# Kernel optimization log

Measured on AMD Instinct MI355X. Metric: run time of the kernel, lower is better.

Reference implementation:

```python
import jax, jax.numpy as jnp
import numpy as np

ALPHA = 0.2        # LeakyReLU negative slope in EEGGraphAttentionLayer
NEG_BIG = -9e15    # zero_vec value used before softmax

B, N, F_IN, H = 32, 1024, 512, 512


def setup_inputs() -> dict:
    key = jax.random.key(0)
    k1, k2, k3, k4 = jax.random.split(key, 4)
    context = jax.random.normal(k1, (B, N, F_IN), dtype=jnp.float32)
    adj = jax.random.randint(k2, (B, N, N), 0, 2, dtype=jnp.int32)
    w = jax.random.normal(k3, (F_IN, H), dtype=jnp.float32) * (1.414 / np.sqrt(F_IN))
    a = jax.random.normal(k4, (2 * H, 1), dtype=jnp.float32) * (1.414 / np.sqrt(2 * H))
    return {"context": context, "adj": adj, "w": w, "a": a}


def reference(context, adj, w, a):
    # context: (B, N, F), adj: (B, N, N), w: (F, H), a: (2H, 1)
    # All num_pers=16 heads share the identical att module, so the mean over
    # num_pers of identical tensors equals a single application (same math).
    context = context.reshape(adj.shape[0], adj.shape[1], -1)
    Wh = jnp.einsum('bnf,fh->bnh', context, w)            # (B, N, H)
    a1, a2 = a[:H, 0], a[H:, 0]                            # (H,), (H,)
    f1 = Wh @ a1                                           # (B, N) -> source index i
    f2 = Wh @ a2                                           # (B, N) -> target index j
    # e[b,i,j] = leakyrelu(f1[b,i] + f2[b,j]); avoids the explicit N x N x 2H tensor
    e = jax.nn.leaky_relu(f1[:, :, None] + f2[:, None, :], negative_slope=ALPHA)
    e = jnp.where(adj > 0, e, NEG_BIG)
    attention = jax.nn.softmax(e, axis=-1)                 # softmax over dim=1 of (N,N)
    # F.dropout is a no-op in eval mode; epsilon=None, ctx_mask=None paths skipped.
    return jax.nn.softplus(attention)
```

## Files before the change

kernel.cpp:

```cpp
#include <hip/hip_runtime.h>
#include <math.h>

#define ALPHA 0.2f

constexpr int B = 32, N = 1024, F_IN = 512, H = 512;

typedef float f32x4 __attribute__((ext_vector_type(4)));

__global__ __launch_bounds__(64) void u_kernel(const float* __restrict__ w,
                                               const float* __restrict__ a,
                                               float* __restrict__ u) {
    const int f = blockIdx.x;
    const int l = threadIdx.x;
    const float* wrow = w + (size_t)f * H;
    float s1 = 0.f, s2 = 0.f;
#pragma unroll
    for (int it = 0; it < H / 64; ++it) {
        const int h = l + it * 64;
        const float wv = wrow[h];
        s1 += wv * a[h];
        s2 += wv * a[h + H];
    }
#pragma unroll
    for (int off = 32; off > 0; off >>= 1) {
        s1 += __shfl_xor(s1, off, 64);
        s2 += __shfl_xor(s2, off, 64);
    }
    if (l == 0) { u[f] = s1; u[f + F_IN] = s2; }
}

__global__ __launch_bounds__(256) void f_kernel(const float* __restrict__ ctx,
                                                const float* __restrict__ u,
                                                float* __restrict__ f1,
                                                float* __restrict__ f2) {
    const int wave = threadIdx.x >> 6;
    const int lane = threadIdx.x & 63;
    const int row  = blockIdx.x * 4 + wave;

    const float4* u1p = (const float4*)u;
    const float4* u2p = (const float4*)(u + F_IN);
    const float4 u1a = u1p[lane * 2],     u1b = u1p[lane * 2 + 1];
    const float4 u2a = u2p[lane * 2],     u2b = u2p[lane * 2 + 1];

    const float4* c4 = (const float4*)(ctx + (size_t)row * F_IN);
    const float4 ca = c4[lane * 2], cb = c4[lane * 2 + 1];

    float s1 = ca.x * u1a.x + ca.y * u1a.y + ca.z * u1a.z + ca.w * u1a.w
             + cb.x * u1b.x + cb.y * u1b.y + cb.z * u1b.z + cb.w * u1b.w;
    float s2 = ca.x * u2a.x + ca.y * u2a.y + ca.z * u2a.z + ca.w * u2a.w
             + cb.x * u2b.x + cb.y * u2b.y + cb.z * u2b.z + cb.w * u2b.w;

#pragma unroll
    for (int off = 32; off > 0; off >>= 1) {
        s1 += __shfl_xor(s1, off, 64);
        s2 += __shfl_xor(s2, off, 64);
    }
    if (lane == 0) { f1[row] = s1; f2[row] = s2; }
}

__device__ __forceinline__ float softplus01(float z) {
    const float z2 = z * z;
    const float t  = fmaf(z2, -5.2083335e-3f, 0.125f);
    return fmaf(z2, t, fmaf(z, 0.5f, 0.69314718f));
}

__global__ __launch_bounds__(256) void attn_kernel(const int* __restrict__ adj,
                                                   const float* __restrict__ f1,
                                                   const float* __restrict__ f2,
                                                   float* __restrict__ out) {
    const int wave = threadIdx.x >> 6;
    const int lane = threadIdx.x & 63;
    const int row  = blockIdx.x * 4 + wave;
    const int b    = row >> 10;

    const int4*   arow = (const int4*)(adj + (size_t)row * N);
    const float4* f2b  = (const float4*)(f2 + (size_t)b * N);
    const float   fi   = f1[row];

    int4   am[4];
    float4 fv[4];
#pragma unroll
    for (int k = 0; k < 4; ++k) {
        am[k] = arow[k * 64 + lane];
        fv[k] = f2b[k * 64 + lane];
    }

    float p[16];
    float s = 0.f;
#pragma unroll
    for (int k = 0; k < 4; ++k) {
        const float f0 = fv[k].x, f1v = fv[k].y, f2v = fv[k].z, f3v = fv[k].w;
        float e0 = fi + f0;  e0 = e0 > 0.f ? e0 : ALPHA * e0;
        float e1 = fi + f1v; e1 = e1 > 0.f ? e1 : ALPHA * e1;
        float e2 = fi + f2v; e2 = e2 > 0.f ? e2 : ALPHA * e2;
        float e3 = fi + f3v; e3 = e3 > 0.f ? e3 : ALPHA * e3;
        const float q0 = (am[k].x > 0) ? __expf(e0) : 0.f;
        const float q1 = (am[k].y > 0) ? __expf(e1) : 0.f;
        const float q2 = (am[k].z > 0) ? __expf(e2) : 0.f;
        const float q3 = (am[k].w > 0) ? __expf(e3) : 0.f;
        p[k * 4 + 0] = q0; p[k * 4 + 1] = q1; p[k * 4 + 2] = q2; p[k * 4 + 3] = q3;
        s += (q0 + q1) + (q2 + q3);
    }

#pragma unroll
    for (int off = 32; off > 0; off >>= 1)
        s += __shfl_xor(s, off, 64);
    const float inv = (s > 0.f) ? (1.0f / s) : 0.f;

    f32x4* orow = (f32x4*)(out + (size_t)row * N);
#pragma unroll
    for (int k = 0; k < 4; ++k) {
        f32x4 o;
        o.x = softplus01(p[k * 4 + 0] * inv);
        o.y = softplus01(p[k * 4 + 1] * inv);
        o.z = softplus01(p[k * 4 + 2] * inv);
        o.w = softplus01(p[k * 4 + 3] * inv);
        __builtin_nontemporal_store(o, orow + k * 64 + lane);
    }
}

extern "C" void kernel_launch(void* const* d_in, const int* in_sizes, int n_in,
                              void* d_out, int out_size, void* d_ws, size_t ws_size,
                              hipStream_t stream) {
    const float* ctx = (const float*)d_in[0];
    const int*   adj = (const int*)d_in[1];
    const float* w   = (const float*)d_in[2];
    const float* a   = (const float*)d_in[3];
    float* out = (float*)d_out;

    float* u  = (float*)d_ws;
    float* f1 = u + 2 * F_IN;
    float* f2 = f1 + B * N;

    u_kernel<<<F_IN, 64, 0, stream>>>(w, a, u);
    f_kernel<<<(B * N) / 4, 256, 0, stream>>>(ctx, u, f1, f2);
    attn_kernel<<<(B * N) / 4, 256, 0, stream>>>(adj, f1, f2, out);
}
```

Measured before the change: 59.65 us.

## Fuse f-projection and attention kernels into persistent grid with global barrier

```diff
diff --git a/kernel.cpp b/kernel.cpp
--- a/kernel.cpp
+++ b/kernel.cpp
@@ -4,12 +4,18 @@
 #define ALPHA 0.2f
 
 constexpr int B = 32, N = 1024, F_IN = 512, H = 512;
+constexpr int GRID = 512, BLK = 256;
+constexpr int ROWS_PER_BLOCK = (B * N) / GRID;
+constexpr int ROWS_PER_WAVE  = ROWS_PER_BLOCK / 4;
 
 typedef float f32x4 __attribute__((ext_vector_type(4)));
 
+
 __global__ __launch_bounds__(64) void u_kernel(const float* __restrict__ w,
                                                const float* __restrict__ a,
-                                               float* __restrict__ u) {
+                                               float* __restrict__ u,
+                                               int* __restrict__ bar) {
+    if (blockIdx.x == 0 && threadIdx.x == 0) { bar[0] = 0; bar[1] = 0; }
     const int f = blockIdx.x;
     const int l = threadIdx.x;
     const float* wrow = w + (size_t)f * H;
@@ -29,93 +35,114 @@
     if (l == 0) { u[f] = s1; u[f + F_IN] = s2; }
 }
 
-__global__ __launch_bounds__(256) void f_kernel(const float* __restrict__ ctx,
-                                                const float* __restrict__ u,
-                                                float* __restrict__ f1,
-                                                float* __restrict__ f2) {
-    const int wave = threadIdx.x >> 6;
-    const int lane = threadIdx.x & 63;
-    const int row  = blockIdx.x * 4 + wave;
-
-    const float4* u1p = (const float4*)u;
-    const float4* u2p = (const float4*)(u + F_IN);
-    const float4 u1a = u1p[lane * 2],     u1b = u1p[lane * 2 + 1];
-    const float4 u2a = u2p[lane * 2],     u2b = u2p[lane * 2 + 1];
-
-    const float4* c4 = (const float4*)(ctx + (size_t)row * F_IN);
-    const float4 ca = c4[lane * 2], cb = c4[lane * 2 + 1];
-
-    float s1 = ca.x * u1a.x + ca.y * u1a.y + ca.z * u1a.z + ca.w * u1a.w
-             + cb.x * u1b.x + cb.y * u1b.y + cb.z * u1b.z + cb.w * u1b.w;
-    float s2 = ca.x * u2a.x + ca.y * u2a.y + ca.z * u2a.z + ca.w * u2a.w
-             + cb.x * u2b.x + cb.y * u2b.y + cb.z * u2b.z + cb.w * u2b.w;
-
-#pragma unroll
-    for (int off = 32; off > 0; off >>= 1) {
-        s1 += __shfl_xor(s1, off, 64);
-        s2 += __shfl_xor(s2, off, 64);
-    }
-    if (lane == 0) { f1[row] = s1; f2[row] = s2; }
-}
-
 __device__ __forceinline__ float softplus01(float z) {
     const float z2 = z * z;
     const float t  = fmaf(z2, -5.2083335e-3f, 0.125f);
     return fmaf(z2, t, fmaf(z, 0.5f, 0.69314718f));
 }
 
-__global__ __launch_bounds__(256) void attn_kernel(const int* __restrict__ adj,
-                                                   const float* __restrict__ f1,
-                                                   const float* __restrict__ f2,
-                                                   float* __restrict__ out) {
+__global__ __launch_bounds__(BLK, 2) void fused_kernel(
+        const float* __restrict__ ctx, const int* __restrict__ adj,
+        const float* __restrict__ u,   float* __restrict__ f2,
+        int* __restrict__ bar,         float* __restrict__ out) {
     const int wave = threadIdx.x >> 6;
     const int lane = threadIdx.x & 63;
-    const int row  = blockIdx.x * 4 + wave;
-    const int b    = row >> 10;
+    const int baseRow = blockIdx.x * ROWS_PER_BLOCK + wave * ROWS_PER_WAVE;
 
-    const int4*   arow = (const int4*)(adj + (size_t)row * N);
-    const float4* f2b  = (const float4*)(f2 + (size_t)b * N);
-    const float   fi   = f1[row];
-
-    int4   am[4];
-    float4 fv[4];
+    float f1r[ROWS_PER_WAVE];
+    {
+        const float4* u1p = (const float4*)u;
+        const float4* u2p = (const float4*)(u + F_IN);
+        const float4 u1a = u1p[lane * 2], u1b = u1p[lane * 2 + 1];
+        const float4 u2a = u2p[lane * 2], u2b = u2p[lane * 2 + 1];
 #pragma unroll
-    for (int k = 0; k < 4; ++k) {
-        am[k] = arow[k * 64 + lane];
-        fv[k] = f2b[k * 64 + lane];
+        for (int i = 0; i < ROWS_PER_WAVE; ++i) {
+            const int row = baseRow + i;
+            const float4* c4 = (const float4*)(ctx + (size_t)row * F_IN);
+            const float4 ca = c4[lane * 2], cb = c4[lane * 2 + 1];
+            float s1 = ca.x * u1a.x + ca.y * u1a.y + ca.z * u1a.z + ca.w * u1a.w
+                     + cb.x * u1b.x + cb.y * u1b.y + cb.z * u1b.z + cb.w * u1b.w;
+            float s2 = ca.x * u2a.x + ca.y * u2a.y + ca.z * u2a.z + ca.w * u2a.w
+                     + cb.x * u2b.x + cb.y * u2b.y + cb.z * u2b.z + cb.w * u2b.w;
+#pragma unroll
+            for (int off = 32; off > 0; off >>= 1) {
+                s1 += __shfl_xor(s1, off, 64);
+                s2 += __shfl_xor(s2, off, 64);
+            }
+            f1r[i] = s1;
+            if (lane == 0) f2[row] = s2;
+        }
     }
 
-    float p[16];
-    float s = 0.f;
+    int4 amn[4];
+    {
+        const int4* arow0 = (const int4*)(adj + (size_t)baseRow * N);
 #pragma unroll
-    for (int k = 0; k < 4; ++k) {
-        const float f0 = fv[k].x, f1v = fv[k].y, f2v = fv[k].z, f3v = fv[k].w;
-        float e0 = fi + f0;  e0 = e0 > 0.f ? e0 : ALPHA * e0;
-        float e1 = fi + f1v; e1 = e1 > 0.f ? e1 : ALPHA * e1;
-        float e2 = fi + f2v; e2 = e2 > 0.f ? e2 : ALPHA * e2;
-        float e3 = fi + f3v; e3 = e3 > 0.f ? e3 : ALPHA * e3;
-        const float q0 = (am[k].x > 0) ? __expf(e0) : 0.f;
-        const float q1 = (am[k].y > 0) ? __expf(e1) : 0.f;
-        const float q2 = (am[k].z > 0) ? __expf(e2) : 0.f;
-        const float q3 = (am[k].w > 0) ? __expf(e3) : 0.f;
-        p[k * 4 + 0] = q0; p[k * 4 + 1] = q1; p[k * 4 + 2] = q2; p[k * 4 + 3] = q3;
-        s += (q0 + q1) + (q2 + q3);
+        for (int k = 0; k < 4; ++k) amn[k] = arow0[k * 64 + lane];
     }
 
+    __syncthreads();
+    if (threadIdx.x == 0) {
+        __builtin_amdgcn_fence(__ATOMIC_RELEASE, "agent");
+        if (__hip_atomic_fetch_add(&bar[0], 1, __ATOMIC_ACQ_REL,
+                                   __HIP_MEMORY_SCOPE_AGENT) == GRID - 1)
+            __hip_atomic_store(&bar[1], 1, __ATOMIC_RELEASE,
+                               __HIP_MEMORY_SCOPE_AGENT);
+        while (__hip_atomic_load(&bar[1], __ATOMIC_ACQUIRE,
+                                 __HIP_MEMORY_SCOPE_AGENT) == 0)
+            __builtin_amdgcn_s_sleep(8);
+    }
+    __syncthreads();
+    __builtin_amdgcn_fence(__ATOMIC_ACQUIRE, "agent");
+
+    const int b = baseRow >> 10;
+    const f32x4* f2b = (const f32x4*)(f2 + (size_t)b * N);
 #pragma unroll
-    for (int off = 32; off > 0; off >>= 1)
-        s += __shfl_xor(s, off, 64);
-    const float inv = (s > 0.f) ? (1.0f / s) : 0.f;
+    for (int i = 0; i < ROWS_PER_WAVE; ++i) {
+        const int row = baseRow + i;
+        int4 am[4];
+#pragma unroll
+        for (int k = 0; k < 4; ++k) am[k] = amn[k];
+        if (i < ROWS_PER_WAVE - 1) {
+            const int4* arown = (const int4*)(adj + (size_t)(row + 1) * N);
+#pragma unroll
+            for (int k = 0; k < 4; ++k) amn[k] = arown[k * 64 + lane];
+        }
 
-    f32x4* orow = (f32x4*)(out + (size_t)row * N);
+        const float fi = f1r[i];
+        float p[16];
+        float s = 0.f;
 #pragma unroll
-    for (int k = 0; k < 4; ++k) {
-        f32x4 o;
-        o.x = softplus01(p[k * 4 + 0] * inv);
-        o.y = softplus01(p[k * 4 + 1] * inv);
-        o.z = softplus01(p[k * 4 + 2] * inv);
-        o.w = softplus01(p[k * 4 + 3] * inv);
-        __builtin_nontemporal_store(o, orow + k * 64 + lane);
+        for (int k = 0; k < 4; ++k) {
+            const f32x4 fv = f2b[k * 64 + lane];
+            float e0 = fi + fv.x; e0 = e0 > 0.f ? e0 : ALPHA * e0;
+            float e1 = fi + fv.y; e1 = e1 > 0.f ? e1 : ALPHA * e1;
+            float e2 = fi + fv.z; e2 = e2 > 0.f ? e2 : ALPHA * e2;
+            float e3 = fi + fv.w; e3 = e3 > 0.f ? e3 : ALPHA * e3;
+            const float q0 = (am[k].x > 0) ? __expf(e0) : 0.f;
+            const float q1 = (am[k].y > 0) ? __expf(e1) : 0.f;
+            const float q2 = (am[k].z > 0) ? __expf(e2) : 0.f;
+            const float q3 = (am[k].w > 0) ? __expf(e3) : 0.f;
+            p[k * 4 + 0] = q0; p[k * 4 + 1] = q1;
+            p[k * 4 + 2] = q2; p[k * 4 + 3] = q3;
+            s += (q0 + q1) + (q2 + q3);
+        }
+
+#pragma unroll
+        for (int off = 32; off > 0; off >>= 1)
+            s += __shfl_xor(s, off, 64);
+        const float inv = (s > 0.f) ? (1.0f / s) : 0.f;
+
+        f32x4* orow = (f32x4*)(out + (size_t)row * N);
+#pragma unroll
+        for (int k = 0; k < 4; ++k) {
+            f32x4 o;
+            o.x = softplus01(p[k * 4 + 0] * inv);
+            o.y = softplus01(p[k * 4 + 1] * inv);
+            o.z = softplus01(p[k * 4 + 2] * inv);
+            o.w = softplus01(p[k * 4 + 3] * inv);
+            __builtin_nontemporal_store(o, orow + k * 64 + lane);
+        }
     }
 }
 
@@ -128,11 +155,10 @@
     const float* a   = (const float*)d_in[3];
     float* out = (float*)d_out;
 
-    float* u  = (float*)d_ws;
-    float* f1 = u + 2 * F_IN;
-    float* f2 = f1 + B * N;
+    float* u   = (float*)d_ws;
+    float* f2  = u + 2 * F_IN;
+    int*   bar = (int*)(f2 + B * N);
 
-    u_kernel<<<F_IN, 64, 0, stream>>>(w, a, u);
-    f_kernel<<<(B * N) / 4, 256, 0, stream>>>(ctx, u, f1, f2);
-    attn_kernel<<<(B * N) / 4, 256, 0, stream>>>(adj, f1, f2, out);
+    u_kernel<<<F_IN, 64, 0, stream>>>(w, a, u, bar);
+    fused_kernel<<<GRID, BLK, 0, stream>>>(ctx, adj, u, f2, bar, out);
 }
```

Result: slower. 132.4 us (+121.9%).
